# Performance work log

Measured on AMD Instinct MI355X. Metric: run time of the kernel, lower is better.

## Reference

```python
import jax, jax.numpy as jnp
import numpy as np

N_VERT = 1000          # num_of_vertices; x has 3*N_VERT rows
B = 32                 # batch
IN_DIM = 64
OUT_DIMS = [64, 64, 64]


def setup_inputs() -> dict:
    key = jax.random.key(0)
    ks = jax.random.split(key, 8)
    threeN = 3 * N_VERT
    x = jax.random.normal(ks[0], (threeN, B, IN_DIM), dtype=jnp.float32)
    # dense (normalized-ish) adjacency over the localized spatio-temporal graph
    adj = jax.random.uniform(ks[1], (threeN, threeN), dtype=jnp.float32) / threeN
    inp = {"x": x, "adj": adj}
    in_d = IN_DIM
    for i, out_d in enumerate(OUT_DIMS):
        # torch Linear(in_d, 2*out_d): store as [in_d, 2*out_d] for x @ W + b
        scale = 1.0 / np.sqrt(in_d)
        inp[f"W{i}"] = jax.random.uniform(ks[2 + 2 * i], (in_d, 2 * out_d),
                                          minval=-scale, maxval=scale, dtype=jnp.float32)
        inp[f"b{i}"] = jax.random.uniform(ks[3 + 2 * i], (2 * out_d,),
                                          minval=-scale, maxval=scale, dtype=jnp.float32)
        in_d = out_d
    return inp


def _gcn_glu(adj, x, W, b, out_dim):
    # aggregate: [3N,3N] x [3N,B,C] -> [3N,B,C]
    h = jnp.einsum('nm,mbc->nbc', adj, x)
    lr = h @ W + b                       # [3N,B,2*out]
    lhs, rhs = lr[..., :out_dim], lr[..., out_dim:]
    return lhs * jax.nn.sigmoid(rhs)     # GLU


def reference(x, adj, W0, b0, W1, b1, W2, b2):
    n = x.shape[0] // 3
    Ws = [(W0, b0), (W1, b1), (W2, b2)]
    mids = []
    h = x
    for (W, b), out_d in zip(Ws, OUT_DIMS):
        h = _gcn_glu(adj, h, W, b, out_d)
        mids.append(h[n:2 * n])          # middle time-step slice [N,B,out]
    return jnp.max(jnp.stack(mids, axis=0), axis=0)  # [N,B,out]
```

## Files before the change

kernel.cpp:

```cpp
#include <hip/hip_runtime.h>
#include <stdint.h>
#include <math.h>

#define NV   3000
#define MP   3072
#define NBC  2048
#define NMID 1000

typedef unsigned short u16;
typedef short  s8vec __attribute__((ext_vector_type(8)));
typedef float  f4vec __attribute__((ext_vector_type(4)));


__device__ __forceinline__ u16 f2b(float f) {
  union { float f; unsigned int u; } v; v.f = f;
  unsigned int r = v.u + 0x7FFFu + ((v.u >> 16) & 1u);
  return (u16)(r >> 16);
}
__device__ __forceinline__ float b2f(u16 u) {
  union { unsigned int u; float f; } v; v.u = ((unsigned int)u) << 16;
  return v.f;
}

__device__ __forceinline__ void gload16(const void* g, void* l) {
  __builtin_amdgcn_global_load_lds(
      (const __attribute__((address_space(1))) void*)g,
      (__attribute__((address_space(3))) void*)l, 16, 0, 0);
}

__global__ void k_conv_adj(const float* __restrict__ adj,
                           u16* __restrict__ adjt) {
  __shared__ __align__(16) u16 tb[64][80];
  const int bx = blockIdx.x;
  const int by = blockIdx.y;
  const int t  = threadIdx.x;

  {
    const int rl = t >> 2, quad = t & 3;
    const int r  = by * 64 + rl;
    const bool rok = (r < NV);
#pragma unroll
    for (int i = 0; i < 4; ++i) {
      int c = bx * 64 + quad * 16 + i * 4;
      float4 f = {0.f, 0.f, 0.f, 0.f};
      if (rok && c < NV) f = *(const float4*)(adj + (size_t)r * NV + c);
      ushort4 o;
      o.x = f2b(f.x); o.y = f2b(f.y); o.z = f2b(f.z); o.w = f2b(f.w);
      *(ushort4*)&tb[rl][quad * 16 + i * 4] = o;
    }
  }
  __syncthreads();

  {
#pragma unroll
    for (int h = 0; h < 2; ++h) {
      int chunk = t * 2 + h;
      int sel  = chunk >> 8;
      int g    = (chunk >> 6) & 3;
      int lane = chunk & 63;
      int row  = g * 16 + (lane & 15);
      int col  = sel * 32 + (lane >> 4) * 8;
      s8vec v = *(const s8vec*)&tb[row][col];
      size_t dst = ((size_t)(by * 96 + bx * 2 + sel) * 4 + g) * 512 + lane * 8;
      *(s8vec*)(adjt + dst) = v;
    }
  }
}

__global__ void k_conv_x(const float* __restrict__ x,
                         u16* __restrict__ xt) {
  __shared__ __align__(16) u16 tb[64][72];
  int t  = threadIdx.x;
  int k0 = blockIdx.x * 64;
  int n0 = blockIdx.y * 64;
  int kl = t >> 4, ch = t & 15;
#pragma unroll
  for (int r = 0; r < 4; ++r) {
    int k = k0 + kl + r * 16;
    float4 f = {0.f, 0.f, 0.f, 0.f};
    if (k < NV) f = *(const float4*)(x + (size_t)k * NBC + n0 + ch * 4);
    tb[ch * 4 + 0][kl + r * 16] = f2b(f.x);
    tb[ch * 4 + 1][kl + r * 16] = f2b(f.y);
    tb[ch * 4 + 2][kl + r * 16] = f2b(f.z);
    tb[ch * 4 + 3][kl + r * 16] = f2b(f.w);
  }
  __syncthreads();
  int nl = t >> 4, kc = t & 15;
#pragma unroll
  for (int r = 0; r < 4; ++r) {
    int n = n0 + nl + r * 16;
    int k = k0 + kc * 4;
    ushort4 o;
    o.x = tb[nl + r * 16][kc * 4 + 0];
    o.y = tb[nl + r * 16][kc * 4 + 1];
    o.z = tb[nl + r * 16][kc * 4 + 2];
    o.w = tb[nl + r * 16][kc * 4 + 3];
    int nt = n >> 7, g = (n >> 4) & 7, lr = n & 15;
    int kk = k >> 5, hi = (k >> 3) & 3, j = k & 7;
    size_t dst = ((size_t)(nt * 96 + kk) * 8 + g) * 512 +
                 (size_t)(hi * 16 + lr) * 8 + j;
    *(ushort4*)(xt + dst) = o;
  }
}

__global__ void k_conv_w(const float* __restrict__ W0,
                         const float* __restrict__ W1,
                         const float* __restrict__ W2,
                         u16* __restrict__ Wt) {
  int e = blockIdx.x * 256 + threadIdx.x;
  const float* W = (e < 8192) ? W0 : (e < 16384) ? W1 : W2;
  int r  = e & 8191;
  int kk = r >> 12, g = (r >> 9) & 7, ln = (r >> 3) & 63, jj = r & 7;
  int c = kk * 32 + (ln >> 4) * 8 + jj;
  int j = g * 16 + (ln & 15);
  Wt[e] = f2b(W[c * 128 + j]);
}

__global__ __launch_bounds__(256, 2) void k_gemm(
    const u16* __restrict__ At,
    const u16* __restrict__ Xt,
    u16* __restrict__ C0,
    u16* __restrict__ C1,
    int m64base,
    int nmt,
    int crow0,
    int chunk) {
  __shared__ __align__(16) u16 S[3 * 6144];

  const int bid = blockIdx.x;
  const int swz = (bid & 7) * chunk + (bid >> 3);
  const int nt  = swz & 15;
  const int mk  = swz >> 4;
  const int ks  = (mk >= nmt) ? 1 : 0;
  const int mt  = mk - ks * nmt;
  const int kt0 = ks * 48;

  const int tid  = threadIdx.x;
  const int w    = tid >> 6;
  const int lane = tid & 63;
  const int wr   = w >> 1;
  const int wc   = w & 1;

  const int c0 = w * 3;
  const u16* asrc[3];
#pragma unroll
  for (int i = 0; i < 3; ++i) {
    int c = c0 + i;
    int m64 = m64base + mt * 3 + (c >> 2);
    asrc[i] = At + ((size_t)(m64 * 96 + kt0) * 4 + (c & 3)) * 512 + lane * 8;
  }
  const u16* bsrc = Xt + ((size_t)(nt * 96 + kt0) * 8 + wc * 4) * 512 + lane * 8;

  f4vec acc[6][4];
#pragma unroll
  for (int i = 0; i < 6; ++i)
#pragma unroll
    for (int j = 0; j < 4; ++j) acc[i][j] = (f4vec){0.f, 0.f, 0.f, 0.f};

  s8vec breg[2][4];

  auto stageA = [&](int buf, int t) {
    u16* d = S + buf * 6144 + c0 * 512;
#pragma unroll
    for (int i = 0; i < 3; ++i)
      gload16(asrc[i] + (size_t)t * 2048, d + i * 512);
  };
  auto loadB = [&](int set, int t) {
#pragma unroll
    for (int ni = 0; ni < 4; ++ni)
      breg[set][ni] = *(const s8vec*)(bsrc + (size_t)t * 4096 + ni * 512);
  };
  auto compute = [&](int buf, int set) {
    const u16* Ab = S + buf * 6144 + (wr * 6) * 512 + lane * 8;
    s8vec a[6];
#pragma unroll
    for (int mi = 0; mi < 6; ++mi)
      a[mi] = *(const s8vec*)(Ab + mi * 512);
#pragma unroll
    for (int mi = 0; mi < 6; ++mi)
#pragma unroll
      for (int ni = 0; ni < 4; ++ni)
        acc[mi][ni] = __builtin_amdgcn_mfma_f32_16x16x32_bf16(
            a[mi], breg[set][ni], acc[mi][ni], 0, 0, 0);
  };

  stageA(0, 0);
  loadB(0, 0);
  stageA(1, 1);

#pragma unroll 1
  for (int t = 0; t < 42; t += 6) {
#pragma unroll
    for (int u = 0; u < 6; ++u) {
      asm volatile("s_waitcnt vmcnt(3)" ::: "memory");
      loadB((u + 1) & 1, t + u + 1);
      asm volatile("s_barrier" ::: "memory");
      stageA((u + 2) % 3, t + u + 2);
      compute(u % 3, u & 1);
    }
  }
  asm volatile("s_waitcnt vmcnt(3)" ::: "memory");
  loadB(1, 43);
  asm volatile("s_barrier" ::: "memory");
  stageA(2, 44);
  compute(0, 0);
  asm volatile("s_waitcnt vmcnt(3)" ::: "memory");
  loadB(0, 44);
  asm volatile("s_barrier" ::: "memory");
  stageA(0, 45);
  compute(1, 1);
  asm volatile("s_waitcnt vmcnt(3)" ::: "memory");
  loadB(1, 45);
  asm volatile("s_barrier" ::: "memory");
  stageA(1, 46);
  compute(2, 0);
  asm volatile("s_waitcnt vmcnt(3)" ::: "memory");
  loadB(0, 46);
  asm volatile("s_barrier" ::: "memory");
  stageA(2, 47);
  compute(0, 1);
  asm volatile("s_waitcnt vmcnt(3)" ::: "memory");
  loadB(1, 47);
  asm volatile("s_barrier" ::: "memory");
  compute(1, 0);
  asm volatile("s_waitcnt vmcnt(0)" ::: "memory");
  asm volatile("s_barrier" ::: "memory");
  compute(2, 1);

  u16* Cs = ks ? C1 : C0;
  const int rl = lane & 15;
  const int rh = lane >> 4;
  const int mrow0 = m64base * 64 + mt * 192 + wr * 96 - crow0;
#pragma unroll
  for (int mi = 0; mi < 6; ++mi)
#pragma unroll
    for (int ni = 0; ni < 4; ++ni) {
      int grow = mrow0 + mi * 16 + rh * 4;
      int gcol = nt * 128 + wc * 64 + ni * 16 + rl;
      u16* cp = Cs + (size_t)grow * NBC + gcol;
      cp[0 * NBC] = f2b(acc[mi][ni][0]);
      cp[1 * NBC] = f2b(acc[mi][ni][1]);
      cp[2 * NBC] = f2b(acc[mi][ni][2]);
      cp[3 * NBC] = f2b(acc[mi][ni][3]);
    }
}

template <int LAYER0, int WRITEX>
__global__ __launch_bounds__(256) void k_layerB(
    const u16* __restrict__ H0,
    const u16* __restrict__ H1,
    const u16* __restrict__ Wt,
    const float* __restrict__ bias,
    u16* __restrict__ xt,
    float* __restrict__ out,
    int vt0) {
  __shared__ __align__(16) u16 Hs[2][2][8][64][8];

  const int vt = vt0 + blockIdx.x;
  const int b  = blockIdx.y;
  const int v0 = vt * 128;
  const int t  = threadIdx.x;

#pragma unroll
  for (int h = 0; h < 2; ++h) {
    const u16* H = h ? H1 : H0;
#pragma unroll
    for (int q = 0; q < 4; ++q) {
      int id = q * 256 + t;
      int v  = id >> 3;
      int cc = (id & 7) * 8;
      s8vec hh = *(const s8vec*)(H + (size_t)(v0 + v) * NBC + b * 64 + cc);
      int kk = cc >> 5, g = v >> 4, ln = ((cc >> 3) & 3) * 16 + (v & 15);
      *(s8vec*)&Hs[h][kk][g][ln][0] = hh;
    }
  }
  __syncthreads();

  const int w    = t >> 6;
  const int lane = t & 63;
  const int wvh  = w >> 1;
  const int wc   = w & 1;

  s8vec bf[4][2];
#pragma unroll
  for (int ni = 0; ni < 4; ++ni) {
    int g = (ni < 2) ? (wc * 2 + ni) : (4 + wc * 2 + (ni - 2));
#pragma unroll
    for (int kk = 0; kk < 2; ++kk)
      bf[ni][kk] = *(const s8vec*)(Wt + ((size_t)(kk * 8 + g) * 64 + lane) * 8);
  }

  f4vec acc[4][4];
#pragma unroll
  for (int i = 0; i < 4; ++i)
#pragma unroll
    for (int j = 0; j < 4; ++j) acc[i][j] = (f4vec){0.f, 0.f, 0.f, 0.f};

#pragma unroll
  for (int h = 0; h < 2; ++h)
#pragma unroll
    for (int kk = 0; kk < 2; ++kk) {
      s8vec a[4];
#pragma unroll
      for (int mi = 0; mi < 4; ++mi)
        a[mi] = *(const s8vec*)&Hs[h][kk][wvh * 4 + mi][lane][0];
#pragma unroll
      for (int mi = 0; mi < 4; ++mi)
#pragma unroll
        for (int ni = 0; ni < 4; ++ni)
          acc[mi][ni] = __builtin_amdgcn_mfma_f32_16x16x32_bf16(
              a[mi], bf[ni][kk], acc[mi][ni], 0, 0, 0);
    }

  const int lr = lane & 15;
  const int rh = lane >> 4;
#pragma unroll
  for (int mi = 0; mi < 4; ++mi) {
    const int vbase = v0 + wvh * 64 + mi * 16 + rh * 4;
#pragma unroll
    for (int np = 0; np < 2; ++np) {
      const int j  = wc * 32 + np * 16 + lr;
      const float bl = bias[j];
      const float bh = bias[j + 64];
      float vals[4];
#pragma unroll
      for (int r = 0; r < 4; ++r) {
        float lo = acc[mi][np][r] + bl;
        float hi = acc[mi][np + 2][r] + bh;
        float gv = lo / (1.0f + __expf(-hi));
        vals[r] = ((vbase + r) < NV) ? gv : 0.0f;
      }
#pragma unroll
      for (int r = 0; r < 4; ++r) {
        int vg = vbase + r;
        if (vg >= NMID && vg < 2 * NMID) {
          size_t oi = (size_t)(vg - NMID) * NBC + b * 64 + j;
          if (LAYER0) out[oi] = vals[r];
          else        out[oi] = fmaxf(out[oi], vals[r]);
        }
      }
      if (WRITEX) {
        int n   = b * 64 + j;
        int nt  = n >> 7, g2 = (n >> 4) & 7, ln2 = n & 15;
        int kk2 = vbase >> 5, hi2 = (vbase >> 3) & 3, jj0 = vbase & 7;
        ushort4 o;
        o.x = f2b(vals[0]); o.y = f2b(vals[1]);
        o.z = f2b(vals[2]); o.w = f2b(vals[3]);
        size_t dst = ((size_t)(nt * 96 + kk2) * 8 + g2) * 512 +
                     (size_t)(hi2 * 16 + ln2) * 8 + jj0;
        *(ushort4*)(xt + dst) = o;
      }
    }
  }
}

extern "C" void kernel_launch(void* const* d_in, const int* in_sizes, int n_in,
                              void* d_out, int out_size, void* d_ws, size_t ws_size,
                              hipStream_t stream) {
  const float* x   = (const float*)d_in[0];
  const float* adj = (const float*)d_in[1];
  const float* W0  = (const float*)d_in[2];
  const float* b0  = (const float*)d_in[3];
  const float* W1  = (const float*)d_in[4];
  const float* b1  = (const float*)d_in[5];
  const float* W2  = (const float*)d_in[6];
  const float* b2  = (const float*)d_in[7];
  float* out = (float*)d_out;

  char* ws = (char*)d_ws;
  u16* adjt = (u16*)ws;
  u16* xa   = (u16*)(ws + 18874368);
  u16* xb   = (u16*)(ws + 18874368 + 12582912);
  u16* hb   = (u16*)(ws + 18874368 + 2 * 12582912);
  u16* Wt   = (u16*)(ws + 18874368 + 3 * 12582912);

  k_conv_adj<<<dim3(48, 48), 256, 0, stream>>>(adj, adjt);
  k_conv_x<<<dim3(48, 32), 256, 0, stream>>>(x, xa);
  k_conv_w<<<96, 256, 0, stream>>>(W0, W1, W2, Wt);

  k_gemm<<<512, 256, 0, stream>>>(adjt, xa, hb, xb, 0, 16, 0, 64);
  k_layerB<1, 1><<<dim3(24, 32), 256, 0, stream>>>(hb, xb, Wt, b0, xa, out, 0);
  k_gemm<<<512, 256, 0, stream>>>(adjt, xa, hb, xb, 0, 16, 0, 64);
  k_layerB<0, 1><<<dim3(24, 32), 256, 0, stream>>>(hb, xb, Wt + 8192, b1, xa, out, 0);
  k_gemm<<<192, 256, 0, stream>>>(adjt, xa, hb, xb, 14, 6, 896, 24);
  k_layerB<0, 0><<<dim3(9, 32), 256, 0, stream>>>(
      hb - (size_t)896 * NBC, xb - (size_t)896 * NBC, Wt + 16384, b2, xa, out, 7);
}
```

Baseline: 182.6 us.

## Halve GEMM M-tile to 96 rows with 64-deep K steps and double grid

```diff
diff --git a/kernel.cpp b/kernel.cpp
--- a/kernel.cpp
+++ b/kernel.cpp
@@ -116,12 +116,12 @@
   Wt[e] = f2b(W[c * 128 + j]);
 }
 
-__global__ __launch_bounds__(256, 2) void k_gemm(
+__global__ __launch_bounds__(256, 4) void k_gemm(
     const u16* __restrict__ At,
     const u16* __restrict__ Xt,
     u16* __restrict__ C0,
     u16* __restrict__ C1,
-    int m64base,
+    int m16base,
     int nmt,
     int crow0,
     int chunk) {
@@ -138,50 +138,57 @@
   const int tid  = threadIdx.x;
   const int w    = tid >> 6;
   const int lane = tid & 63;
-  const int wr   = w >> 1;
-  const int wc   = w & 1;
-
-  const int c0 = w * 3;
+  const int wc   = w;
+
+  const int rb16 = m16base + mt * 6;
   const u16* asrc[3];
 #pragma unroll
   for (int i = 0; i < 3; ++i) {
-    int c = c0 + i;
-    int m64 = m64base + mt * 3 + (c >> 2);
-    asrc[i] = At + ((size_t)(m64 * 96 + kt0) * 4 + (c & 3)) * 512 + lane * 8;
-  }
-  const u16* bsrc = Xt + ((size_t)(nt * 96 + kt0) * 8 + wc * 4) * 512 + lane * 8;
-
-  f4vec acc[6][4];
+    int c   = w * 3 + i;
+    int r16 = rb16 + (c >> 1);
+    int m64 = r16 >> 2, g = r16 & 3;
+    asrc[i] = At + ((size_t)(m64 * 96 + kt0) * 4 + g) * 512 +
+              (c & 1) * 2048 + lane * 8;
+  }
+  const u16* bsrc = Xt + ((size_t)(nt * 96 + kt0) * 8 + wc * 2) * 512 + lane * 8;
+
+  f4vec acc[6][2];
 #pragma unroll
   for (int i = 0; i < 6; ++i)
 #pragma unroll
-    for (int j = 0; j < 4; ++j) acc[i][j] = (f4vec){0.f, 0.f, 0.f, 0.f};
-
-  s8vec breg[2][4];
-
-  auto stageA = [&](int buf, int t) {
-    u16* d = S + buf * 6144 + c0 * 512;
+    for (int j = 0; j < 2; ++j) acc[i][j] = (f4vec){0.f, 0.f, 0.f, 0.f};
+
+  s8vec breg[2][2][2];
+
+  auto stageA = [&](int buf, int s) {
+    u16* d = S + buf * 6144 + (w * 3) * 512;
 #pragma unroll
     for (int i = 0; i < 3; ++i)
-      gload16(asrc[i] + (size_t)t * 2048, d + i * 512);
+      gload16(asrc[i] + (size_t)s * 4096, d + i * 512);
   };
-  auto loadB = [&](int set, int t) {
-#pragma unroll
-    for (int ni = 0; ni < 4; ++ni)
-      breg[set][ni] = *(const s8vec*)(bsrc + (size_t)t * 4096 + ni * 512);
+  auto loadB = [&](int set, int s) {
+#pragma unroll
+    for (int kh = 0; kh < 2; ++kh)
+#pragma unroll
+      for (int ni = 0; ni < 2; ++ni)
+        breg[set][kh][ni] =
+            *(const s8vec*)(bsrc + (size_t)s * 8192 + kh * 4096 + ni * 512);
   };
   auto compute = [&](int buf, int set) {
-    const u16* Ab = S + buf * 6144 + (wr * 6) * 512 + lane * 8;
-    s8vec a[6];
-#pragma unroll
-    for (int mi = 0; mi < 6; ++mi)
-      a[mi] = *(const s8vec*)(Ab + mi * 512);
-#pragma unroll
-    for (int mi = 0; mi < 6; ++mi)
-#pragma unroll
-      for (int ni = 0; ni < 4; ++ni)
-        acc[mi][ni] = __builtin_amdgcn_mfma_f32_16x16x32_bf16(
-            a[mi], breg[set][ni], acc[mi][ni], 0, 0, 0);
+    const u16* Ab = S + buf * 6144 + lane * 8;
+#pragma unroll
+    for (int kh = 0; kh < 2; ++kh) {
+      s8vec a[6];
+#pragma unroll
+      for (int mi = 0; mi < 6; ++mi)
+        a[mi] = *(const s8vec*)(Ab + (mi * 2 + kh) * 512);
+#pragma unroll
+      for (int mi = 0; mi < 6; ++mi)
+#pragma unroll
+        for (int ni = 0; ni < 2; ++ni)
+          acc[mi][ni] = __builtin_amdgcn_mfma_f32_16x16x32_bf16(
+              a[mi], breg[set][kh][ni], acc[mi][ni], 0, 0, 0);
+    }
   };
 
   stageA(0, 0);
@@ -189,38 +196,39 @@
   stageA(1, 1);
 
 #pragma unroll 1
-  for (int t = 0; t < 42; t += 6) {
+  for (int sb = 0; sb < 18; sb += 6) {
 #pragma unroll
     for (int u = 0; u < 6; ++u) {
+      const int s = sb + u;
       asm volatile("s_waitcnt vmcnt(3)" ::: "memory");
-      loadB((u + 1) & 1, t + u + 1);
+      loadB((u + 1) & 1, s + 1);
       asm volatile("s_barrier" ::: "memory");
-      stageA((u + 2) % 3, t + u + 2);
+      stageA((u + 2) % 3, s + 2);
       compute(u % 3, u & 1);
     }
   }
   asm volatile("s_waitcnt vmcnt(3)" ::: "memory");
-  loadB(1, 43);
-  asm volatile("s_barrier" ::: "memory");
-  stageA(2, 44);
+  loadB(1, 19);
+  asm volatile("s_barrier" ::: "memory");
+  stageA(2, 20);
   compute(0, 0);
   asm volatile("s_waitcnt vmcnt(3)" ::: "memory");
-  loadB(0, 44);
-  asm volatile("s_barrier" ::: "memory");
-  stageA(0, 45);
+  loadB(0, 20);
+  asm volatile("s_barrier" ::: "memory");
+  stageA(0, 21);
   compute(1, 1);
   asm volatile("s_waitcnt vmcnt(3)" ::: "memory");
-  loadB(1, 45);
-  asm volatile("s_barrier" ::: "memory");
-  stageA(1, 46);
+  loadB(1, 21);
+  asm volatile("s_barrier" ::: "memory");
+  stageA(1, 22);
   compute(2, 0);
   asm volatile("s_waitcnt vmcnt(3)" ::: "memory");
-  loadB(0, 46);
-  asm volatile("s_barrier" ::: "memory");
-  stageA(2, 47);
+  loadB(0, 22);
+  asm volatile("s_barrier" ::: "memory");
+  stageA(2, 23);
   compute(0, 1);
   asm volatile("s_waitcnt vmcnt(3)" ::: "memory");
-  loadB(1, 47);
+  loadB(1, 23);
   asm volatile("s_barrier" ::: "memory");
   compute(1, 0);
   asm volatile("s_waitcnt vmcnt(0)" ::: "memory");
@@ -230,13 +238,13 @@
   u16* Cs = ks ? C1 : C0;
   const int rl = lane & 15;
   const int rh = lane >> 4;
-  const int mrow0 = m64base * 64 + mt * 192 + wr * 96 - crow0;
+  const int mrow0 = rb16 * 16 - crow0;
 #pragma unroll
   for (int mi = 0; mi < 6; ++mi)
 #pragma unroll
-    for (int ni = 0; ni < 4; ++ni) {
+    for (int ni = 0; ni < 2; ++ni) {
       int grow = mrow0 + mi * 16 + rh * 4;
-      int gcol = nt * 128 + wc * 64 + ni * 16 + rl;
+      int gcol = nt * 128 + wc * 32 + ni * 16 + rl;
       u16* cp = Cs + (size_t)grow * NBC + gcol;
       cp[0 * NBC] = f2b(acc[mi][ni][0]);
       cp[1 * NBC] = f2b(acc[mi][ni][1]);
@@ -378,11 +386,11 @@
   k_conv_x<<<dim3(48, 32), 256, 0, stream>>>(x, xa);
   k_conv_w<<<96, 256, 0, stream>>>(W0, W1, W2, Wt);
 
-  k_gemm<<<512, 256, 0, stream>>>(adjt, xa, hb, xb, 0, 16, 0, 64);
+  k_gemm<<<1024, 256, 0, stream>>>(adjt, xa, hb, xb, 0, 32, 0, 128);
   k_layerB<1, 1><<<dim3(24, 32), 256, 0, stream>>>(hb, xb, Wt, b0, xa, out, 0);
-  k_gemm<<<512, 256, 0, stream>>>(adjt, xa, hb, xb, 0, 16, 0, 64);
+  k_gemm<<<1024, 256, 0, stream>>>(adjt, xa, hb, xb, 0, 32, 0, 128);
   k_layerB<0, 1><<<dim3(24, 32), 256, 0, stream>>>(hb, xb, Wt + 8192, b1, xa, out, 0);
-  k_gemm<<<192, 256, 0, stream>>>(adjt, xa, hb, xb, 14, 6, 896, 24);
+  k_gemm<<<384, 256, 0, stream>>>(adjt, xa, hb, xb, 56, 12, 896, 48);
   k_layerB<0, 0><<<dim3(9, 32), 256, 0, stream>>>(
       hb - (size_t)896 * NBC, xb - (size_t)896 * NBC, Wt + 16384, b2, xa, out, 7);
 }
```

Result: slower. 198.2 us (+8.6%).
